# Optimization experiments

Hardware: AMD Instinct MI355X
Metric: run time of the kernel (lower is better)

Reference implementation:

```python
import math
import jax, jax.numpy as jnp
import numpy as np


def setup_inputs() -> dict:
    key = jax.random.key(0)
    ks = jax.random.split(key, 6)
    B, L, d_model = 8, 4096, 512
    s = 1.0 / math.sqrt(d_model)
    inp = {
        "x": jax.random.normal(ks[0], (B, L, d_model), dtype=jnp.float32),
        "Wq": jax.random.normal(ks[1], (d_model, d_model), dtype=jnp.float32) * s,
        "bq": jnp.zeros((d_model,), jnp.float32),
        "Wk": jax.random.normal(ks[2], (d_model, d_model), dtype=jnp.float32) * s,
        "bk": jnp.zeros((d_model,), jnp.float32),
        "Wv": jax.random.normal(ks[3], (d_model, d_model), dtype=jnp.float32) * s,
        "bv": jnp.zeros((d_model,), jnp.float32),
        "Wo": jax.random.normal(ks[4], (d_model, d_model), dtype=jnp.float32) * s,
        "bo": jnp.zeros((d_model,), jnp.float32),
    }
    return inp


N_HEADS = 8
FACTOR = 1


def reference(x, Wq, bq, Wk, bk, Wv, bv, Wo, bo):
    B, L, d_model = x.shape
    H = N_HEADS
    D = d_model // H
    # projections (torch Linear: x @ W.T + b), reshape to (B,H,L,D)
    def proj(W, b):
        y = jnp.einsum("bld,ed->ble", x, W) + b
        return y.reshape(B, L, H, D).transpose(0, 2, 1, 3)
    q = proj(Wq, bq)
    k = proj(Wk, bk)
    v = proj(Wv, bv)
    # FFT autocorrelation along time axis (axis=2)
    q_f = jnp.fft.rfft(q, axis=2)
    k_f = jnp.fft.rfft(k, axis=2)
    corr = jnp.fft.irfft(q_f * jnp.conj(k_f), n=L, axis=2)  # (B,H,L,D)
    k_top = max(1, int(FACTOR * math.log(L + 1)))
    k_top = min(k_top, L)
    corr_mean = corr.mean(axis=-1)  # (B,H,L)
    top_vals, top_idx = jax.lax.top_k(corr_mean, k_top)  # (B,H,k)
    weights = jax.nn.softmax(top_vals, axis=-1)  # (B,H,k)
    t = jnp.arange(L).reshape(1, 1, 1, L)
    idx = (t + top_idx[..., None]) % L  # (B,H,k,L)
    # gather rolled V per selected lag: (B,H,k,L,D)
    v_exp = jnp.broadcast_to(v[:, :, None], (B, H, k_top, L, D))
    gathered = jnp.take_along_axis(v_exp, idx[..., None], axis=3)
    out = jnp.einsum("bhkld,bhk->bhld", gathered, weights)
    out = out.transpose(0, 2, 1, 3).reshape(B, L, d_model)
    # dropout=0.0 (eval): identity
    return jnp.einsum("bld,ed->ble", out, Wo) + bo
```

## Files before the change

### kernel.cpp

```cpp
#include <hip/hip_runtime.h>
#include <cstdint>
#include <cstddef>

#define AS1 __attribute__((address_space(1)))
#define AS3 __attribute__((address_space(3)))

using half8  = __attribute__((ext_vector_type(8))) _Float16;
using half4v = __attribute__((ext_vector_type(4))) _Float16;
using half2v = __attribute__((ext_vector_type(2))) _Float16;
using f32x4  = __attribute__((ext_vector_type(4))) float;

__global__ void prep_all_kernel(const float* __restrict__ x,
                                const float* __restrict__ Wq, const float* __restrict__ Wk,
                                const float* __restrict__ Wv, const float* __restrict__ Wo,
                                const float* __restrict__ bq, const float* __restrict__ bk,
                                const float* __restrict__ bv,
                                _Float16* __restrict__ xh, _Float16* __restrict__ Bt,
                                _Float16* __restrict__ WoH,
                                float2* __restrict__ tw, float* __restrict__ bias) {
    const int bid = blockIdx.x;
    const int tid = threadIdx.x;
    if (bid < 16384) {
        int i = (bid * 256 + tid) * 4;
        float4 v = *(const float4*)(x + i);
        half4v h;
        h[0] = (_Float16)v.x; h[1] = (_Float16)v.y;
        h[2] = (_Float16)v.z; h[3] = (_Float16)v.w;
        *(half4v*)(xh + i) = h;
    } else if (bid < 19456) {
        int i = (bid - 16384) * 256 + tid;
        int e = i >> 9, k = i & 511;
        int proj = e >> 9, er = e & 511;
        const float* W = (proj == 0) ? Wq : ((proj == 1) ? Wk : Wv);
        Bt[i] = (_Float16)W[er * 512 + k];
    } else if (bid < 20480) {
        int i = (bid - 19456) * 256 + tid;
        WoH[i] = (_Float16)Wo[i];
    } else if (bid < 20496) {
        int p = (bid - 20480) * 256 + tid;
        double th = -2.0 * 3.14159265358979323846 * (double)p / 4096.0;
        tw[p] = make_float2((float)cos(th), (float)sin(th));
    } else {
        int i = (bid - 20496) * 256 + tid;
        bias[i] = (i < 512) ? bq[i] : ((i < 1024) ? bk[i - 512] : bv[i - 1024]);
    }
}

template <int MODE>
__global__ __launch_bounds__(256, 4) void gemm_f16_kernel(
    const _Float16* __restrict__ A, const _Float16* __restrict__ Bt,
    const float* __restrict__ bias,
    _Float16* __restrict__ qT, _Float16* __restrict__ kT,
    _Float16* __restrict__ vout, float* __restrict__ Cout)
{
    constexpr int NBLK  = (MODE == 0) ? 12 : 4;
    constexpr int PERXCD = (MODE == 0) ? 384 : 128;
    __shared__ _Float16 As[128 * 32];
    __shared__ _Float16 Bs[128 * 32];

    const int gi = (blockIdx.x & 7) * PERXCD + (blockIdx.x >> 3);
    const int mb = gi / NBLK;
    const int nb = gi - mb * NBLK;
    const int m0 = mb * 128, n0 = nb * 128;
    const int tid = threadIdx.x;
    const int wave = tid >> 6, lane = tid & 63;
    const int wm = (wave & 1) * 64, wn = (wave >> 1) * 64;
    const int lane15 = lane & 15, quad = lane >> 4;
    const int srow = lane >> 2;
    const int scolB = (lane & 3) * 16;

    f32x4 acc[4][4];
#pragma unroll
    for (int mi = 0; mi < 4; mi++)
#pragma unroll
        for (int ni = 0; ni < 4; ni++)
#pragma unroll
            for (int r = 0; r < 4; r++) acc[mi][ni][r] = 0.f;

    for (int kt = 0; kt < 16; kt++) {
        const int kg = kt * 32;
        __syncthreads();
#pragma unroll
        for (int i = 0; i < 2; i++) {
            const int rb = wave * 32 + i * 16;
            const char* ga = (const char*)A  + ((size_t)(m0 + rb + srow)) * 1024 + kg * 2 + scolB;
            const char* gb = (const char*)Bt + ((size_t)(n0 + rb + srow)) * 1024 + kg * 2 + scolB;
            __builtin_amdgcn_global_load_lds((const AS1 void*)ga, (AS3 void*)((char*)As + rb * 64), 16, 0, 0);
            __builtin_amdgcn_global_load_lds((const AS1 void*)gb, (AS3 void*)((char*)Bs + rb * 64), 16, 0, 0);
        }
        __syncthreads();
        half8 af[4], bfr[4];
#pragma unroll
        for (int mi = 0; mi < 4; mi++)
            af[mi] = *(const half8*)((const char*)As + (wm + mi * 16 + lane15) * 64 + quad * 16);
#pragma unroll
        for (int ni = 0; ni < 4; ni++)
            bfr[ni] = *(const half8*)((const char*)Bs + (wn + ni * 16 + lane15) * 64 + quad * 16);
#pragma unroll
        for (int mi = 0; mi < 4; mi++)
#pragma unroll
            for (int ni = 0; ni < 4; ni++)
                acc[mi][ni] = __builtin_amdgcn_mfma_f32_16x16x32_f16(af[mi], bfr[ni], acc[mi][ni], 0, 0, 0);
    }

    if (MODE == 1) {
#pragma unroll
        for (int mi = 0; mi < 4; mi++)
#pragma unroll
            for (int ni = 0; ni < 4; ni++) {
                const int n = n0 + wn + ni * 16 + lane15;
                const float bb = bias[n];
#pragma unroll
                for (int r = 0; r < 4; r++) {
                    const int m = m0 + wm + mi * 16 + quad * 4 + r;
                    Cout[(size_t)m * 512 + n] = acc[mi][ni][r] + bb;
                }
            }
        return;
    }
    const int proj = n0 >> 9;
    if (proj == 2) {
#pragma unroll
        for (int mi = 0; mi < 4; mi++)
#pragma unroll
            for (int ni = 0; ni < 4; ni++) {
                const int n = n0 + wn + ni * 16 + lane15;
                const int er = n - 1024, h = er >> 6, d = er & 63;
                const float bb = bias[n];
#pragma unroll
                for (int r = 0; r < 4; r++) {
                    const int m = m0 + wm + mi * 16 + quad * 4 + r;
                    const int b = m >> 12, l = m & 4095;
                    vout[((size_t)((b * 8 + h) * 4096 + l)) * 64 + d] = (_Float16)(acc[mi][ni][r] + bb);
                }
            }
        return;
    }
    _Float16* dst = (proj == 0) ? qT : kT;
    const int b = m0 >> 12;
    const int lbase = (m0 & 4095) + wm + quad * 4;
#pragma unroll
    for (int mi = 0; mi < 4; mi++)
#pragma unroll
        for (int ni = 0; ni < 4; ni++) {
            const int e = n0 + wn + ni * 16 + lane15;
            const int er = e & 511, h = er >> 6, d = er & 63;
            const float bb = bias[e];
            half4v o;
            o[0] = (_Float16)(acc[mi][ni][0] + bb);
            o[1] = (_Float16)(acc[mi][ni][1] + bb);
            o[2] = (_Float16)(acc[mi][ni][2] + bb);
            o[3] = (_Float16)(acc[mi][ni][3] + bb);
            *(half4v*)(dst + ((size_t)((b * 8 + h) * 64 + d)) * 4096 + lbase + mi * 16) = o;
        }
}

__device__ __forceinline__ float2 cmul(float2 a, float2 b) {
    return make_float2(a.x * b.x - a.y * b.y, a.x * b.y + a.y * b.x);
}
__device__ __forceinline__ float2 cmulc(float2 a, float cr, float ci) {
    return make_float2(a.x * cr - a.y * ci, a.x * ci + a.y * cr);
}
__device__ __forceinline__ int swz(int i) { return i ^ ((i >> 4) & 15); }

__device__ __forceinline__ void dft16(float2 x[16]) {
    constexpr float wc[10] = {1.f, 0.92387953f, 0.70710678f, 0.38268343f, 0.f,
                              0.f, -0.70710678f, 0.f, 0.f, -0.92387953f};
    constexpr float wsn[10] = {0.f, -0.38268343f, -0.70710678f, -0.92387953f, -1.f,
                               0.f, -0.70710678f, 0.f, 0.f, 0.38268343f};
    float2 t[16];
#pragma unroll
    for (int u = 0; u < 4; u++) {
        const float2 a = x[u], b = x[u + 4], c = x[u + 8], d = x[u + 12];
        const float2 Ea = make_float2(a.x + c.x, a.y + c.y);
        const float2 Oa = make_float2(a.x - c.x, a.y - c.y);
        const float2 Eb = make_float2(b.x + d.x, b.y + d.y);
        const float2 Ob = make_float2(b.x - d.x, b.y - d.y);
        const float2 y0 = make_float2(Ea.x + Eb.x, Ea.y + Eb.y);
        const float2 y1 = make_float2(Oa.x + Ob.y, Oa.y - Ob.x);
        const float2 y2 = make_float2(Ea.x - Eb.x, Ea.y - Eb.y);
        const float2 y3 = make_float2(Oa.x - Ob.y, Oa.y + Ob.x);
        t[4 * u + 0] = y0;
        t[4 * u + 1] = cmulc(y1, wc[u * 1], wsn[u * 1]);
        t[4 * u + 2] = cmulc(y2, wc[u * 2], wsn[u * 2]);
        t[4 * u + 3] = cmulc(y3, wc[u * 3], wsn[u * 3]);
    }
#pragma unroll
    for (int v = 0; v < 4; v++) {
        const float2 a = t[v], b = t[v + 4], c = t[v + 8], d = t[v + 12];
        const float2 Ea = make_float2(a.x + c.x, a.y + c.y);
        const float2 Oa = make_float2(a.x - c.x, a.y - c.y);
        const float2 Eb = make_float2(b.x + d.x, b.y + d.y);
        const float2 Ob = make_float2(b.x - d.x, b.y - d.y);
        x[v]      = make_float2(Ea.x + Eb.x, Ea.y + Eb.y);
        x[v + 4]  = make_float2(Oa.x + Ob.y, Oa.y - Ob.x);
        x[v + 8]  = make_float2(Ea.x - Eb.x, Ea.y - Eb.y);
        x[v + 12] = make_float2(Oa.x - Ob.y, Oa.y + Ob.x);
    }
}

__device__ __forceinline__ void fft4096_r16(float2* buf, const float2* __restrict__ tw,
                                            int tid, float2 (&x)[16]) {
    __syncthreads();
#pragma unroll
    for (int j = 0; j < 16; j++) x[j] = buf[swz(tid + 256 * j)];
    __syncthreads();
    dft16(x);
    buf[swz(16 * tid)] = x[0];
#pragma unroll
    for (int m = 1; m < 16; m++) buf[swz(16 * tid + m)] = cmul(x[m], tw[tid * m]);
    __syncthreads();
#pragma unroll
    for (int j = 0; j < 16; j++) x[j] = buf[swz(tid + 256 * j)];
    __syncthreads();
    dft16(x);
    {
        const int q = tid & 15, p = tid >> 4;
        const int base = q + 256 * p;
        buf[swz(base)] = x[0];
#pragma unroll
        for (int m = 1; m < 16; m++)
            buf[swz(base + 16 * m)] = cmul(x[m], tw[(p * m) << 4]);
    }
    __syncthreads();
#pragma unroll
    for (int j = 0; j < 16; j++) x[j] = buf[swz(tid + 256 * j)];
    __syncthreads();
    dft16(x);
#pragma unroll
    for (int m = 0; m < 16; m++) buf[swz(tid + 256 * m)] = x[m];
    __syncthreads();
}

__global__ __launch_bounds__(256) void fft_partial_kernel(
    const _Float16* __restrict__ qT, const _Float16* __restrict__ kT,
    const float2* __restrict__ tw, float2* __restrict__ spec)
{
    __shared__ float2 buf[4096];
    const int tid = threadIdx.x;
    const int bh = blockIdx.x >> 4, chunk = blockIdx.x & 15;
    float sx[16], sy[16];
#pragma unroll
    for (int i = 0; i < 16; i++) { sx[i] = 0.f; sy[i] = 0.f; }
    const _Float16* qb = qT + (size_t)bh * 64 * 4096;
    const _Float16* kb = kT + (size_t)bh * 64 * 4096;
    float2 x[16];
    for (int dd = 0; dd < 4; dd++) {
        const int d = chunk * 4 + dd;
#pragma unroll
        for (int i = 0; i < 2; i++) {
            const int t0 = 2048 * i + tid * 8;
            const half8 fq = *(const half8*)(qb + d * 4096 + t0);
            const half8 fk = *(const half8*)(kb + d * 4096 + t0);
#pragma unroll
            for (int j = 0; j < 8; j++)
                buf[swz(t0 + j)] = make_float2((float)fq[j], (float)fk[j]);
        }
        fft4096_r16(buf, tw, tid, x);
#pragma unroll
        for (int i = 0; i < 16; i++) {
            const int f = tid + 256 * i;
            const float2 Zf = x[i];
            const float2 Zm = buf[swz((4096 - f) & 4095)];
            const float Qr  = 0.5f * (Zf.x + Zm.x);
            const float Qi  = 0.5f * (Zf.y - Zm.y);
            const float cKr = 0.5f * (Zf.y + Zm.y);
            const float cKi = 0.5f * (Zf.x - Zm.x);
            sx[i] += Qr * cKr - Qi * cKi;
            sy[i] += Qr * cKi + Qi * cKr;
        }
        __syncthreads();
    }
    float2* out = spec + (size_t)blockIdx.x * 4096;
#pragma unroll
    for (int i = 0; i < 16; i++) out[tid + 256 * i] = make_float2(sx[i], sy[i]);
}

__global__ __launch_bounds__(256) void sum_spec_kernel(
    const float4* __restrict__ spec4, float4* __restrict__ ssum4)
{
    const int bh = blockIdx.x >> 3;
    const int i4 = (blockIdx.x & 7) * 256 + threadIdx.x;
    const float4* base = spec4 + (size_t)bh * 16 * 2048 + i4;
    float4 s = make_float4(0.f, 0.f, 0.f, 0.f);
#pragma unroll
    for (int c = 0; c < 16; c++) {
        const float4 v = base[(size_t)c * 2048];
        s.x += v.x; s.y += v.y; s.z += v.z; s.w += v.w;
    }
    s.y = -s.y; s.w = -s.w;
    ssum4[(size_t)bh * 2048 + i4] = s;
}

__global__ __launch_bounds__(256) void reduce_topk_kernel(
    const float2* __restrict__ ssum, const float2* __restrict__ tw,
    int* __restrict__ top_idx, float* __restrict__ top_w)
{
    __shared__ float2 buf[4096];
    __shared__ float wv[4];
    __shared__ int wi[4];
    const int tid = threadIdx.x;
    const int bh = blockIdx.x;
#pragma unroll
    for (int i = 0; i < 16; i++) {
        const int f = tid + 256 * i;
        buf[swz(f)] = ssum[(size_t)bh * 4096 + f];
    }
    float2 x[16];
    fft4096_r16(buf, tw, tid, x);
    float vals[8]; int idxs[8];
    for (int k = 0; k < 8; k++) {
        float best = -3.0e38f; int bi = 0;
#pragma unroll
        for (int i = 0; i < 16; i++) {
            const int f = tid + 256 * i;
            const float c = buf[swz(f)].x;
            if (c > best) { best = c; bi = f; }
        }
#pragma unroll
        for (int off = 32; off > 0; off >>= 1) {
            const float ov = __shfl_down(best, off);
            const int oi = __shfl_down(bi, off);
            if (ov > best || (ov == best && oi < bi)) { best = ov; bi = oi; }
        }
        if ((tid & 63) == 0) { wv[tid >> 6] = best; wi[tid >> 6] = bi; }
        __syncthreads();
        if (tid == 0) {
            best = wv[0]; bi = wi[0];
            for (int w = 1; w < 4; w++) {
                if (wv[w] > best || (wv[w] == best && wi[w] < bi)) { best = wv[w]; bi = wi[w]; }
            }
            vals[k] = best; idxs[k] = bi;
            buf[swz(bi)].x = -3.4e38f;
        }
        __syncthreads();
    }
    if (tid == 0) {
        const float scale = 1.f / (4096.f * 64.f);
        float e[8], s = 0.f;
        const float mx = vals[0] * scale;
        for (int k = 0; k < 8; k++) { e[k] = __expf(vals[k] * scale - mx); s += e[k]; }
        for (int k = 0; k < 8; k++) {
            top_w[bh * 8 + k] = e[k] / s;
            top_idx[bh * 8 + k] = idxs[k];
        }
    }
}

__global__ __launch_bounds__(256) void gather_kernel(
    const half8* __restrict__ v8, const int* __restrict__ top_idx,
    const float* __restrict__ top_w, half8* __restrict__ out8)
{
    const int seq = blockIdx.x;
    const int bh = seq >> 7;
    const int lgrp = seq & 127;
    const int b = bh >> 3, h = bh & 7;
    const int tid = threadIdx.x;
    const int l = lgrp * 32 + (tid >> 3);
    const int d8 = tid & 7;
    int idx[8]; float w[8];
#pragma unroll
    for (int k = 0; k < 8; k++) { idx[k] = top_idx[bh * 8 + k]; w[k] = top_w[bh * 8 + k]; }
    const half8* vb = v8 + (size_t)bh * 4096 * 8;
    float a[8];
#pragma unroll
    for (int j = 0; j < 8; j++) a[j] = 0.f;
#pragma unroll
    for (int k = 0; k < 8; k++) {
        const int ls = (l + idx[k]) & 4095;
        const half8 pv = vb[(size_t)ls * 8 + d8];
#pragma unroll
        for (int j = 0; j < 8; j++) a[j] += w[k] * (float)pv[j];
    }
    half8 o;
#pragma unroll
    for (int j = 0; j < 8; j++) o[j] = (_Float16)a[j];
    out8[((size_t)(b * 4096 + l)) * 64 + h * 8 + d8] = o;
}

extern "C" void kernel_launch(void* const* d_in, const int* in_sizes, int n_in,
                              void* d_out, int out_size, void* d_ws, size_t ws_size,
                              hipStream_t stream) {
    (void)in_sizes; (void)n_in; (void)out_size; (void)ws_size;
    const float* x  = (const float*)d_in[0];
    const float* Wq = (const float*)d_in[1];
    const float* bq = (const float*)d_in[2];
    const float* Wk = (const float*)d_in[3];
    const float* bk = (const float*)d_in[4];
    const float* Wv = (const float*)d_in[5];
    const float* bv = (const float*)d_in[6];
    const float* Wo = (const float*)d_in[7];
    const float* bo = (const float*)d_in[8];
    float* out = (float*)d_out;

    char* ws = (char*)d_ws;
    size_t off = 0;
    auto alloc = [&](size_t bytes) -> void* {
        void* p = ws + off; off += (bytes + 255) & ~(size_t)255; return p;
    };
    _Float16* xh   = (_Float16*)alloc(33554432);
    _Float16* qT   = (_Float16*)alloc(33554432);
    _Float16* kT   = (_Float16*)alloc(33554432);
    _Float16* vbuf = (_Float16*)alloc(33554432);
    float2* spec   = (float2*)alloc(33554432);
    float2* ssum   = (float2*)alloc(2097152);
    _Float16* BtH  = (_Float16*)alloc(1572864);
    _Float16* WoH  = (_Float16*)alloc(524288);
    float* biasQKV = (float*)alloc(6144);
    float2* tw     = (float2*)alloc(32768);
    int*   top_idx = (int*)alloc(2048);
    float* top_w   = (float*)alloc(2048);
    _Float16* out_pre = xh;

    prep_all_kernel<<<20502, 256, 0, stream>>>(x, Wq, Wk, Wv, Wo, bq, bk, bv,
                                               xh, BtH, WoH, tw, biasQKV);
    gemm_f16_kernel<0><<<3072, 256, 0, stream>>>(xh, BtH, biasQKV, qT, kT, vbuf, nullptr);
    fft_partial_kernel<<<1024, 256, 0, stream>>>(qT, kT, tw, spec);
    sum_spec_kernel<<<512, 256, 0, stream>>>((const float4*)spec, (float4*)ssum);
    reduce_topk_kernel<<<64, 256, 0, stream>>>(ssum, tw, top_idx, top_w);
    gather_kernel<<<8192, 256, 0, stream>>>((const half8*)vbuf, top_idx, top_w,
                                            (half8*)out_pre);
    gemm_f16_kernel<1><<<1024, 256, 0, stream>>>(out_pre, WoH, bo, nullptr, nullptr, nullptr, out);
}
```

Before: 333.0 us.

## Use 256x256 GEMM tiles with a 4-stage LDS pipeline and swizzled reads

Result: faster. 319.6 us (-4.0%).

```diff
diff --git a/kernel.cpp b/kernel.cpp
--- a/kernel.cpp
+++ b/kernel.cpp
@@ -47,72 +47,108 @@
 }
 
 template <int MODE>
-__global__ __launch_bounds__(256, 4) void gemm_f16_kernel(
+__global__ __launch_bounds__(512, 2) void gemm_f16_kernel(
     const _Float16* __restrict__ A, const _Float16* __restrict__ Bt,
     const float* __restrict__ bias,
     _Float16* __restrict__ qT, _Float16* __restrict__ kT,
     _Float16* __restrict__ vout, float* __restrict__ Cout)
 {
-    constexpr int NBLK  = (MODE == 0) ? 12 : 4;
-    constexpr int PERXCD = (MODE == 0) ? 384 : 128;
-    __shared__ _Float16 As[128 * 32];
-    __shared__ _Float16 Bs[128 * 32];
+    constexpr int NBLK   = (MODE == 0) ? 6 : 2;
+    constexpr int PERXCD = (MODE == 0) ? 96 : 32;
+    __shared__ _Float16 smem[65536];
 
     const int gi = (blockIdx.x & 7) * PERXCD + (blockIdx.x >> 3);
     const int mb = gi / NBLK;
     const int nb = gi - mb * NBLK;
-    const int m0 = mb * 128, n0 = nb * 128;
+    const int m0 = mb * 256, n0 = nb * 256;
     const int tid = threadIdx.x;
     const int wave = tid >> 6, lane = tid & 63;
-    const int wm = (wave & 1) * 64, wn = (wave >> 1) * 64;
     const int lane15 = lane & 15, quad = lane >> 4;
-    const int srow = lane >> 2;
-    const int scolB = (lane & 3) * 16;
-
-    f32x4 acc[4][4];
-#pragma unroll
-    for (int mi = 0; mi < 4; mi++)
+    const int wmr = (wave >> 2) * 128;
+    const int wnr = (wave & 3) * 64;
+
+    const int row0 = tid >> 2;
+    const int kq   = (tid & 3) ^ ((tid >> 3) & 3);
+    const char* gA0 = (const char*)A  + ((size_t)(m0 + row0)) * 1024 + kq * 16;
+    const char* gA1 = gA0 + (size_t)128 * 1024;
+    const char* gB0 = (const char*)Bt + ((size_t)(n0 + row0)) * 1024 + kq * 16;
+    const char* gB1 = gB0 + (size_t)128 * 1024;
+    const int ldsA0 = wave * 1024;
+    const int ldsA1 = 8192 + wave * 1024;
+    const int ldsB0 = 16384 + wave * 1024;
+    const int ldsB1 = 24576 + wave * 1024;
+
+    const int coloff = ((quad ^ ((lane15 >> 1) & 3)) << 4);
+
+    f32x4 acc[8][4];
+#pragma unroll
+    for (int mi = 0; mi < 8; mi++)
 #pragma unroll
         for (int ni = 0; ni < 4; ni++)
 #pragma unroll
             for (int r = 0; r < 4; r++) acc[mi][ni][r] = 0.f;
 
-    for (int kt = 0; kt < 16; kt++) {
-        const int kg = kt * 32;
-        __syncthreads();
-#pragma unroll
-        for (int i = 0; i < 2; i++) {
-            const int rb = wave * 32 + i * 16;
-            const char* ga = (const char*)A  + ((size_t)(m0 + rb + srow)) * 1024 + kg * 2 + scolB;
-            const char* gb = (const char*)Bt + ((size_t)(n0 + rb + srow)) * 1024 + kg * 2 + scolB;
-            __builtin_amdgcn_global_load_lds((const AS1 void*)ga, (AS3 void*)((char*)As + rb * 64), 16, 0, 0);
-            __builtin_amdgcn_global_load_lds((const AS1 void*)gb, (AS3 void*)((char*)Bs + rb * 64), 16, 0, 0);
-        }
-        __syncthreads();
-        half8 af[4], bfr[4];
-#pragma unroll
-        for (int mi = 0; mi < 4; mi++)
-            af[mi] = *(const half8*)((const char*)As + (wm + mi * 16 + lane15) * 64 + quad * 16);
+    auto STAGE = [&](int slot, int kt) {
+        const int off = kt * 64;
+        char* base = (char*)smem + slot * 32768;
+        __builtin_amdgcn_global_load_lds((const AS1 void*)(gA0 + off), (AS3 void*)(base + ldsA0), 16, 0, 0);
+        __builtin_amdgcn_global_load_lds((const AS1 void*)(gA1 + off), (AS3 void*)(base + ldsA1), 16, 0, 0);
+        __builtin_amdgcn_global_load_lds((const AS1 void*)(gB0 + off), (AS3 void*)(base + ldsB0), 16, 0, 0);
+        __builtin_amdgcn_global_load_lds((const AS1 void*)(gB1 + off), (AS3 void*)(base + ldsB1), 16, 0, 0);
+    };
+    auto COMPUTE = [&](int slot) {
+        const char* ba = (const char*)smem + slot * 32768;
+        const char* bb = ba + 16384;
+        half8 af[8], bf[4];
+#pragma unroll
+        for (int mi = 0; mi < 8; mi++)
+            af[mi] = *(const half8*)(ba + (wmr + mi * 16 + lane15) * 64 + coloff);
 #pragma unroll
         for (int ni = 0; ni < 4; ni++)
-            bfr[ni] = *(const half8*)((const char*)Bs + (wn + ni * 16 + lane15) * 64 + quad * 16);
-#pragma unroll
-        for (int mi = 0; mi < 4; mi++)
+            bf[ni] = *(const half8*)(bb + (wnr + ni * 16 + lane15) * 64 + coloff);
+        __builtin_amdgcn_s_setprio(1);
+#pragma unroll
+        for (int mi = 0; mi < 8; mi++)
 #pragma unroll
             for (int ni = 0; ni < 4; ni++)
-                acc[mi][ni] = __builtin_amdgcn_mfma_f32_16x16x32_f16(af[mi], bfr[ni], acc[mi][ni], 0, 0, 0);
-    }
+                acc[mi][ni] = __builtin_amdgcn_mfma_f32_16x16x32_f16(af[mi], bf[ni], acc[mi][ni], 0, 0, 0);
+        __builtin_amdgcn_s_setprio(0);
+    };
+
+    STAGE(0, 0); STAGE(1, 1); STAGE(2, 2);
+    for (int t = 0; t <= 12; ++t) {
+        STAGE((t + 3) & 3, t + 3);
+        asm volatile("s_waitcnt vmcnt(12)" ::: "memory");
+        __builtin_amdgcn_s_barrier();
+        asm volatile("" ::: "memory");
+        COMPUTE(t & 3);
+        __builtin_amdgcn_s_barrier();
+    }
+    asm volatile("s_waitcnt vmcnt(8)" ::: "memory");
+    __builtin_amdgcn_s_barrier();
+    asm volatile("" ::: "memory");
+    COMPUTE(1);
+    __builtin_amdgcn_s_barrier();
+    asm volatile("s_waitcnt vmcnt(4)" ::: "memory");
+    __builtin_amdgcn_s_barrier();
+    asm volatile("" ::: "memory");
+    COMPUTE(2);
+    __builtin_amdgcn_s_barrier();
+    asm volatile("s_waitcnt vmcnt(0)" ::: "memory");
+    __builtin_amdgcn_s_barrier();
+    asm volatile("" ::: "memory");
+    COMPUTE(3);
 
     if (MODE == 1) {
 #pragma unroll
-        for (int mi = 0; mi < 4; mi++)
+        for (int mi = 0; mi < 8; mi++)
 #pragma unroll
             for (int ni = 0; ni < 4; ni++) {
-                const int n = n0 + wn + ni * 16 + lane15;
+                const int n = n0 + wnr + ni * 16 + lane15;
                 const float bb = bias[n];
 #pragma unroll
                 for (int r = 0; r < 4; r++) {
-                    const int m = m0 + wm + mi * 16 + quad * 4 + r;
+                    const int m = m0 + wmr + mi * 16 + quad * 4 + r;
                     Cout[(size_t)m * 512 + n] = acc[mi][ni][r] + bb;
                 }
             }
@@ -121,15 +157,15 @@
     const int proj = n0 >> 9;
     if (proj == 2) {
 #pragma unroll
-        for (int mi = 0; mi < 4; mi++)
+        for (int mi = 0; mi < 8; mi++)
 #pragma unroll
             for (int ni = 0; ni < 4; ni++) {
-                const int n = n0 + wn + ni * 16 + lane15;
+                const int n = n0 + wnr + ni * 16 + lane15;
                 const int er = n - 1024, h = er >> 6, d = er & 63;
                 const float bb = bias[n];
 #pragma unroll
                 for (int r = 0; r < 4; r++) {
-                    const int m = m0 + wm + mi * 16 + quad * 4 + r;
+                    const int m = m0 + wmr + mi * 16 + quad * 4 + r;
                     const int b = m >> 12, l = m & 4095;
                     vout[((size_t)((b * 8 + h) * 4096 + l)) * 64 + d] = (_Float16)(acc[mi][ni][r] + bb);
                 }
@@ -138,12 +174,12 @@
     }
     _Float16* dst = (proj == 0) ? qT : kT;
     const int b = m0 >> 12;
-    const int lbase = (m0 & 4095) + wm + quad * 4;
-#pragma unroll
-    for (int mi = 0; mi < 4; mi++)
+    const int lbase = (m0 & 4095) + wmr + quad * 4;
+#pragma unroll
+    for (int mi = 0; mi < 8; mi++)
 #pragma unroll
         for (int ni = 0; ni < 4; ni++) {
-            const int e = n0 + wn + ni * 16 + lane15;
+            const int e = n0 + wnr + ni * 16 + lane15;
             const int er = e & 511, h = er >> 6, d = er & 63;
             const float bb = bias[e];
             half4v o;
@@ -414,11 +450,11 @@
 
     prep_all_kernel<<<20502, 256, 0, stream>>>(x, Wq, Wk, Wv, Wo, bq, bk, bv,
                                                xh, BtH, WoH, tw, biasQKV);
-    gemm_f16_kernel<0><<<3072, 256, 0, stream>>>(xh, BtH, biasQKV, qT, kT, vbuf, nullptr);
+    gemm_f16_kernel<0><<<768, 512, 0, stream>>>(xh, BtH, biasQKV, qT, kT, vbuf, nullptr);
     fft_partial_kernel<<<1024, 256, 0, stream>>>(qT, kT, tw, spec);
     sum_spec_kernel<<<512, 256, 0, stream>>>((const float4*)spec, (float4*)ssum);
     reduce_topk_kernel<<<64, 256, 0, stream>>>(ssum, tw, top_idx, top_w);
     gather_kernel<<<8192, 256, 0, stream>>>((const half8*)vbuf, top_idx, top_w,
                                             (half8*)out_pre);
-    gemm_f16_kernel<1><<<1024, 256, 0, stream>>>(out_pre, WoH, bo, nullptr, nullptr, nullptr, out);
-}
+    gemm_f16_kernel<1><<<256, 512, 0, stream>>>(out_pre, WoH, bo, nullptr, nullptr, nullptr, out);
+}
```
